# Performance work log

Measured on AMD Instinct MI355X. Metric: run time of the kernel, lower is better.

The kernel has to match this reference:

```python
import jax, jax.numpy as jnp
import numpy as np


def setup_inputs() -> dict:
    key = jax.random.key(0)
    k1, k2, k3, k4 = jax.random.split(key, 4)
    B, V, F, H, W = 2, 4, 32, 256, 256
    G, GH, GW, GD = 1, 64, 64, 64
    return {
        "feat_maps": jax.random.normal(k1, (B, V, F, H, W), dtype=jnp.float32),
        "RTs": jax.random.normal(k2, (B, V, 3, 4), dtype=jnp.float32),
        "Ks": jax.random.normal(k3, (B, V, 3, 3), dtype=jnp.float32),
        "grids": jax.random.normal(k4, (B, G, 3, GH, GW, GD), dtype=jnp.float32),
    }


def _bilinear_sample(feat, x, y):
    """feat: (F, H, W); x, y: (N,) pixel coords (align_corners=False already applied).
    Zero padding outside image. Returns (F, N)."""
    F_, H, W = feat.shape
    x0 = jnp.floor(x)
    y0 = jnp.floor(y)
    wx1 = x - x0
    wx0 = 1.0 - wx1
    wy1 = y - y0
    wy0 = 1.0 - wy1

    def gather(xi, yi, w):
        valid = (xi >= 0) & (xi <= W - 1) & (yi >= 0) & (yi <= H - 1)
        xc = jnp.clip(xi, 0, W - 1).astype(jnp.int32)
        yc = jnp.clip(yi, 0, H - 1).astype(jnp.int32)
        return feat[:, yc, xc] * (w * valid)[None, :]

    return (gather(x0, y0, wx0 * wy0)
            + gather(x0 + 1.0, y0, wx1 * wy0)
            + gather(x0, y0 + 1.0, wx0 * wy1)
            + gather(x0 + 1.0, y0 + 1.0, wx1 * wy1))


def reference(feat_maps, RTs, Ks, grids):
    B, V, Fd, H, W = feat_maps.shape
    _, G, _, GH, GW, GD = grids.shape
    N = G * GH * GW * GD

    # (B, 3, N) grid points, G-major ordering (matches transpose(1,2).view)
    xyz = jnp.transpose(grids, (0, 2, 1, 3, 4, 5)).reshape(B, 3, N)
    ones = jnp.ones((B, 1, N), dtype=xyz.dtype)
    pts = jnp.concatenate([xyz, ones], axis=1)  # (B, 4, N)

    KRT = jnp.einsum('bvij,bvjk->bvik', Ks, RTs)      # (B, V, 3, 4)
    uvd = jnp.einsum('bvij,bjn->bvin', KRT, pts)      # (B, V, 3, N)
    u = 2.0 * uvd[:, :, 0] / uvd[:, :, 2] / (W - 1.0) - 1.0
    v = 2.0 * uvd[:, :, 1] / uvd[:, :, 2] / (H - 1.0) - 1.0

    # torch grid_sample align_corners=False unnormalization
    x = ((u + 1.0) * W - 1.0) * 0.5
    y = ((v + 1.0) * H - 1.0) * 0.5

    sample_bv = jax.vmap(jax.vmap(_bilinear_sample))  # over B then V
    feat = sample_bv(feat_maps, x, y)                 # (B, V, F, N)

    inv_v = 1.0 / float(V)
    mean = feat.sum(axis=1) * inv_v                   # (B, F, N)
    msq = (feat * feat).sum(axis=1) * inv_v           # (B, F, N)
    var = msq - mean * mean

    out = jnp.concatenate([mean, var], axis=1)        # (B, 2F, N)
    out = out.reshape(B, 2 * Fd, G, GH, GW, GD)
    return jnp.transpose(out, (0, 2, 1, 3, 4, 5))     # (B, G, 2F, GH, GW, GD)
```

## Files before the change

kernel.cpp:

```cpp
#include <hip/hip_runtime.h>
#include <math.h>

#define B_ 2
#define V_ 4
#define F_ 32
#define H_ 256
#define W_ 256
#define N_ 262144

__device__ __forceinline__ void project_f(const float* k, float x, float y,
                                          float z, float& px, float& py) {
#pragma clang fp contract(off)
    float u0 = k[0] * x;  u0 = u0 + k[1] * y;  u0 = u0 + k[2]  * z;  u0 = u0 + k[3];
    float u1 = k[4] * x;  u1 = u1 + k[5] * y;  u1 = u1 + k[6]  * z;  u1 = u1 + k[7];
    float u2 = k[8] * x;  u2 = u2 + k[9] * y;  u2 = u2 + k[10] * z;  u2 = u2 + k[11];
    float uu = 2.0f * u0; uu = uu / u2; uu = uu / 255.0f; uu = uu - 1.0f;
    float vv = 2.0f * u1; vv = vv / u2; vv = vv / 255.0f; vv = vv - 1.0f;
    float tx = uu + 1.0f; tx = tx * 256.0f; tx = tx - 1.0f; px = tx * 0.5f;
    float ty = vv + 1.0f; ty = ty * 256.0f; ty = ty - 1.0f; py = ty * 0.5f;
}

__device__ __forceinline__ void corner_weights_f(float px, float py,
                                                 float& w00, float& w01,
                                                 float& w10, float& w11,
                                                 int& x0, int& x1,
                                                 int& y0, int& y1) {
#pragma clang fp contract(off)
    float x0f = floorf(px), y0f = floorf(py);
    float wx1 = px - x0f, wx0 = 1.0f - wx1;
    float wy1 = py - y0f, wy0 = 1.0f - wy1;
    bool vx0 = (x0f >= 0.0f)  && (x0f <= 255.0f);
    bool vx1 = (x0f >= -1.0f) && (x0f <= 254.0f);
    bool vy0 = (y0f >= 0.0f)  && (y0f <= 255.0f);
    bool vy1 = (y0f >= -1.0f) && (y0f <= 254.0f);
    w00 = (vx0 && vy0) ? wx0 * wy0 : 0.0f;
    w01 = (vx1 && vy0) ? wx1 * wy0 : 0.0f;
    w10 = (vx0 && vy1) ? wx0 * wy1 : 0.0f;
    w11 = (vx1 && vy1) ? wx1 * wy1 : 0.0f;
    x0 = (int)fminf(fmaxf(x0f,        0.0f), 255.0f);
    x1 = (int)fminf(fmaxf(x0f + 1.0f, 0.0f), 255.0f);
    y0 = (int)fminf(fmaxf(y0f,        0.0f), 255.0f);
    y1 = (int)fminf(fmaxf(y0f + 1.0f, 0.0f), 255.0f);
}

__global__ __launch_bounds__(256) void transpose_kernel(
        const float* __restrict__ feat, float* __restrict__ ft) {
    __shared__ float lds[32][257];
    int blk = blockIdx.x;
    int bv = blk >> 8;
    int y  = blk & 255;
    int t  = threadIdx.x;

    size_t base = (size_t)bv * (32 * 65536) + (size_t)y * 256;
#pragma unroll
    for (int f = 0; f < 32; f++) {
        lds[f][t] = feat[base + (size_t)f * 65536 + t];
    }
    __syncthreads();

    size_t obase = ((size_t)bv * 256 + y) * 8192;
#pragma unroll
    for (int k = 0; k < 32; k++) {
        int idx = k * 256 + t;
        ft[obase + idx] = lds[idx & 31][idx >> 5];
    }
}

__global__ __launch_bounds__(256) void sample_kernel(
        const float* __restrict__ ft, const float* __restrict__ RTs,
        const float* __restrict__ Ks, const float* __restrict__ grids,
        float* __restrict__ out) {
    __shared__ float lkrt[4][12];
    __shared__ float sx[4][64];
    __shared__ float sy[4][64];
    __shared__ float smean[32][65];
    __shared__ float svar[32][65];

    int t   = threadIdx.x;
    int blk = blockIdx.x;
    int b   = blk >> 12;
    int n0  = (blk & 4095) << 6;

    if (t < 48) {
#pragma clang fp contract(off)
        int v = t / 12, ij = t % 12, i = ij >> 2, j = ij & 3;
        int bv = b * 4 + v;
        const float* K = Ks + bv * 9;
        const float* R = RTs + bv * 12;
        float acc = K[i * 3 + 0] * R[0 * 4 + j];
        acc = acc + K[i * 3 + 1] * R[1 * 4 + j];
        acc = acc + K[i * 3 + 2] * R[2 * 4 + j];
        lkrt[v][ij] = acc;
    }
    __syncthreads();

    {
        int v = t >> 6, p = t & 63;
        int n = n0 + p;
        size_t gb = (size_t)b * 3 * N_ + n;
        float x = grids[gb];
        float y = grids[gb + N_];
        float z = grids[gb + 2 * (size_t)N_];
        float px, py;
        project_f(lkrt[v], x, y, z, px, py);
        sx[v][p] = px;
        sy[v][p] = py;
    }
    __syncthreads();

    int f = t & 31, g = t >> 5;
    for (int i = 0; i < 8; i++) {
#pragma clang fp contract(off)
        int p = g * 8 + i;
        float accm = 0.0f, accq = 0.0f;
#pragma unroll
        for (int v = 0; v < 4; v++) {
            float px = sx[v][p], py = sy[v][p];
            float w00, w01, w10, w11;
            int x0, x1, y0, y1;
            corner_weights_f(px, py, w00, w01, w10, w11, x0, x1, y0, y1);
            if (w00 + w01 + w10 + w11 != 0.0f) {
                size_t rb = ((size_t)(b * 4 + v)) << 16;
                size_t i00 = ((rb + (size_t)(y0 * 256 + x0)) << 5) + f;
                size_t i01 = ((rb + (size_t)(y0 * 256 + x1)) << 5) + f;
                size_t i10 = ((rb + (size_t)(y1 * 256 + x0)) << 5) + f;
                size_t i11 = ((rb + (size_t)(y1 * 256 + x1)) << 5) + f;
                float s = ft[i00] * w00;
                s = s + ft[i01] * w01;
                s = s + ft[i10] * w10;
                s = s + ft[i11] * w11;
                accm = accm + s;
                float q = s * s;
                accq = accq + q;
            }
        }
        float mean = accm * 0.25f;
        float msq  = accq * 0.25f;
        float mean2 = mean * mean;
        float var   = msq - mean2;
        smean[f][p] = mean;
        svar[f][p]  = var;
    }
    __syncthreads();

    int j = t & 63, c4 = t >> 6;
    size_t ob = (size_t)b * 64 * N_ + n0 + j;
#pragma unroll
    for (int k = 0; k < 16; k++) {
        int c = k * 4 + c4;
        float val = (c < 32) ? smean[c][j] : svar[c - 32][j];
        out[ob + (size_t)c * N_] = val;
    }
}

__global__ __launch_bounds__(256) void naive_kernel(
        const float* __restrict__ feat, const float* __restrict__ RTs,
        const float* __restrict__ Ks, const float* __restrict__ grids,
        float* __restrict__ out) {
#pragma clang fp contract(off)
    size_t idx = (size_t)blockIdx.x * 256 + threadIdx.x;
    int n  = (int)(idx & (N_ - 1));
    int bf = (int)(idx >> 18);
    int f  = bf & 31, b = bf >> 5;

    size_t gb = (size_t)b * 3 * N_ + n;
    float x = grids[gb];
    float y = grids[gb + N_];
    float z = grids[gb + 2 * (size_t)N_];

    float accm = 0.0f, accq = 0.0f;
    for (int v = 0; v < 4; v++) {
        int bv = b * 4 + v;
        const float* K = Ks + bv * 9;
        const float* R = RTs + bv * 12;
        float k[12];
#pragma unroll
        for (int i = 0; i < 3; i++)
#pragma unroll
            for (int j = 0; j < 4; j++) {
                float acc = K[i * 3 + 0] * R[0 * 4 + j];
                acc = acc + K[i * 3 + 1] * R[1 * 4 + j];
                acc = acc + K[i * 3 + 2] * R[2 * 4 + j];
                k[i * 4 + j] = acc;
            }
        float px, py;
        project_f(k, x, y, z, px, py);
        float w00, w01, w10, w11;
        int x0, x1, y0, y1;
        corner_weights_f(px, py, w00, w01, w10, w11, x0, x1, y0, y1);
        if (w00 + w01 + w10 + w11 != 0.0f) {
            size_t fb = ((size_t)bv * 32 + f) * 65536;
            float s = feat[fb + y0 * 256 + x0] * w00;
            s = s + feat[fb + y0 * 256 + x1] * w01;
            s = s + feat[fb + y1 * 256 + x0] * w10;
            s = s + feat[fb + y1 * 256 + x1] * w11;
            accm = accm + s;
            float q = s * s;
            accq = accq + q;
        }
    }
    float mean = accm * 0.25f;
    float msq  = accq * 0.25f;
    float mean2 = mean * mean;
    float var   = msq - mean2;
    size_t ob = ((size_t)b * 64 + f) * N_ + n;
    out[ob] = mean;
    out[ob + 32 * (size_t)N_] = var;
}

extern "C" void kernel_launch(void* const* d_in, const int* in_sizes, int n_in,
                              void* d_out, int out_size, void* d_ws, size_t ws_size,
                              hipStream_t stream) {
    const float* feat  = (const float*)d_in[0];
    const float* RTs   = (const float*)d_in[1];
    const float* Ks    = (const float*)d_in[2];
    const float* grids = (const float*)d_in[3];
    float* out = (float*)d_out;

    const size_t ft_bytes = (size_t)B_ * V_ * H_ * W_ * F_ * sizeof(float);
    if (ws_size >= ft_bytes) {
        float* ft = (float*)d_ws;
        transpose_kernel<<<B_ * V_ * H_, 256, 0, stream>>>(feat, ft);
        sample_kernel<<<(B_ * N_) / 64, 256, 0, stream>>>(ft, RTs, Ks, grids, out);
    } else {
        naive_kernel<<<(B_ * F_ * N_) / 256, 256, 0, stream>>>(feat, RTs, Ks, grids, out);
    }
}
```

Before: 262.8 us.

## Vectorize feature gathers to float4 and precompute corner weights/offsets in LDS

```diff
diff --git a/kernel.cpp b/kernel.cpp
--- a/kernel.cpp
+++ b/kernel.cpp
@@ -71,8 +71,8 @@
         const float* __restrict__ Ks, const float* __restrict__ grids,
         float* __restrict__ out) {
     __shared__ float lkrt[4][12];
-    __shared__ float sx[4][64];
-    __shared__ float sy[4][64];
+    __shared__ __align__(16) float        w4lds[4][64][4];
+    __shared__ __align__(16) unsigned int o4lds[4][64][4];
     __shared__ float smean[32][65];
     __shared__ float svar[32][65];
 
@@ -103,43 +103,58 @@
         float z = grids[gb + 2 * (size_t)N_];
         float px, py;
         project_f(lkrt[v], x, y, z, px, py);
-        sx[v][p] = px;
-        sy[v][p] = py;
-    }
-    __syncthreads();
-
-    int f = t & 31, g = t >> 5;
-    for (int i = 0; i < 8; i++) {
-#pragma clang fp contract(off)
-        int p = g * 8 + i;
-        float accm = 0.0f, accq = 0.0f;
+        float w00, w01, w10, w11;
+        int x0, x1, y0, y1;
+        corner_weights_f(px, py, w00, w01, w10, w11, x0, x1, y0, y1);
+        w4lds[v][p][0] = w00;
+        w4lds[v][p][1] = w01;
+        w4lds[v][p][2] = w10;
+        w4lds[v][p][3] = w11;
+        unsigned int rb = (unsigned int)(b * 4 + v) << 16;
+        o4lds[v][p][0] = (rb + (unsigned int)(y0 * 256 + x0)) << 7;
+        o4lds[v][p][1] = (rb + (unsigned int)(y0 * 256 + x1)) << 7;
+        o4lds[v][p][2] = (rb + (unsigned int)(y1 * 256 + x0)) << 7;
+        o4lds[v][p][3] = (rb + (unsigned int)(y1 * 256 + x1)) << 7;
+    }
+    __syncthreads();
+
+    int ln = t & 7;
+    int sg = t >> 3;
+    const char* ftb = (const char*)ft;
+    unsigned int lnoff = (unsigned int)(ln << 4);
+
+    for (int pass = 0; pass < 2; pass++) {
+#pragma clang fp contract(off)
+        int p = sg + pass * 32;
+        float am0 = 0.0f, am1 = 0.0f, am2 = 0.0f, am3 = 0.0f;
+        float aq0 = 0.0f, aq1 = 0.0f, aq2 = 0.0f, aq3 = 0.0f;
 #pragma unroll
         for (int v = 0; v < 4; v++) {
-            float px = sx[v][p], py = sy[v][p];
-            float w00, w01, w10, w11;
-            int x0, x1, y0, y1;
-            corner_weights_f(px, py, w00, w01, w10, w11, x0, x1, y0, y1);
-            if (w00 + w01 + w10 + w11 != 0.0f) {
-                size_t rb = ((size_t)(b * 4 + v)) << 16;
-                size_t i00 = ((rb + (size_t)(y0 * 256 + x0)) << 5) + f;
-                size_t i01 = ((rb + (size_t)(y0 * 256 + x1)) << 5) + f;
-                size_t i10 = ((rb + (size_t)(y1 * 256 + x0)) << 5) + f;
-                size_t i11 = ((rb + (size_t)(y1 * 256 + x1)) << 5) + f;
-                float s = ft[i00] * w00;
-                s = s + ft[i01] * w01;
-                s = s + ft[i10] * w10;
-                s = s + ft[i11] * w11;
-                accm = accm + s;
-                float q = s * s;
-                accq = accq + q;
+            const float4 w = *(const float4*)w4lds[v][p];
+            const uint4  o = *(const uint4*) o4lds[v][p];
+            float wsum = w.x + w.y;  wsum = wsum + w.z;  wsum = wsum + w.w;
+            if (wsum != 0.0f) {
+                float4 c00 = *(const float4*)(ftb + (o.x + lnoff));
+                float4 c01 = *(const float4*)(ftb + (o.y + lnoff));
+                float4 c10 = *(const float4*)(ftb + (o.z + lnoff));
+                float4 c11 = *(const float4*)(ftb + (o.w + lnoff));
+                float s0 = c00.x * w.x; s0 = s0 + c01.x * w.y; s0 = s0 + c10.x * w.z; s0 = s0 + c11.x * w.w;
+                float s1 = c00.y * w.x; s1 = s1 + c01.y * w.y; s1 = s1 + c10.y * w.z; s1 = s1 + c11.y * w.w;
+                float s2 = c00.z * w.x; s2 = s2 + c01.z * w.y; s2 = s2 + c10.z * w.z; s2 = s2 + c11.z * w.w;
+                float s3 = c00.w * w.x; s3 = s3 + c01.w * w.y; s3 = s3 + c10.w * w.z; s3 = s3 + c11.w * w.w;
+                am0 = am0 + s0;  am1 = am1 + s1;  am2 = am2 + s2;  am3 = am3 + s3;
+                float q0 = s0 * s0, q1 = s1 * s1, q2 = s2 * s2, q3 = s3 * s3;
+                aq0 = aq0 + q0;  aq1 = aq1 + q1;  aq2 = aq2 + q2;  aq3 = aq3 + q3;
             }
         }
-        float mean = accm * 0.25f;
-        float msq  = accq * 0.25f;
-        float mean2 = mean * mean;
-        float var   = msq - mean2;
-        smean[f][p] = mean;
-        svar[f][p]  = var;
+        float m0 = am0 * 0.25f, m1 = am1 * 0.25f, m2 = am2 * 0.25f, m3 = am3 * 0.25f;
+        float e0 = aq0 * 0.25f, e1 = aq1 * 0.25f, e2 = aq2 * 0.25f, e3 = aq3 * 0.25f;
+        float mm0 = m0 * m0, mm1 = m1 * m1, mm2 = m2 * m2, mm3 = m3 * m3;
+        int c = ln << 2;
+        smean[c + 0][p] = m0;  svar[c + 0][p] = e0 - mm0;
+        smean[c + 1][p] = m1;  svar[c + 1][p] = e1 - mm1;
+        smean[c + 2][p] = m2;  svar[c + 2][p] = e2 - mm2;
+        smean[c + 3][p] = m3;  svar[c + 3][p] = e3 - mm3;
     }
     __syncthreads();
 
```

After: 233.1 us. -11.3%, faster.
